# Kernel optimization log

Measured on AMD Instinct MI355X. Metric: run time of the kernel, lower is better.

The kernel has to match this reference:

```python
import jax, jax.numpy as jnp
import numpy as np


def setup_inputs() -> dict:
    key = jax.random.key(0)
    B, T, H, W = 256, 16, 160, 160
    sms = 2
    N = T * (H // sms) * (W // sms)  # 102400 tokens per sample
    k1, _ = jax.random.split(key)
    soft_scores = jax.random.uniform(k1, (B, N), dtype=jnp.float32)
    image_grid_thw = jnp.tile(jnp.array([T, H, W], dtype=jnp.int64), (B, 1))
    return {
        "soft_scores": soft_scores,
        "image_grid_thw": image_grid_thw,
        "spatial_merge_size": sms,
    }


def reference(soft_scores, image_grid_thw, spatial_merge_size,
              lambda_compact=1.0, lambda_tv=1.0, eps=1e-6):
    if soft_scores.ndim == 3:
        soft_scores = soft_scores[..., 0]
    B = soft_scores.shape[0]
    # Uniform grid across the batch (static shapes) -> vectorize over B.
    thw = np.asarray(image_grid_thw)
    t = int(thw[0, 0])
    h = int(thw[0, 1]) // spatial_merge_size
    w = int(thw[0, 2]) // spatial_merge_size
    n = t * h * w

    # s: [B, t, h, w], clamped at 0 like torch clamp_min(0.0)
    s = jnp.maximum(soft_scores[:, :n].astype(jnp.float32).reshape(B, t, h, w), 0.0)
    tot = jnp.maximum(s.sum(axis=(1, 2, 3), keepdims=True), eps)
    p = s / tot  # per-sample normalized distribution

    yy = jnp.linspace(-1.0, 1.0, h, dtype=jnp.float32).reshape(1, 1, h, 1)
    xx = jnp.linspace(-1.0, 1.0, w, dtype=jnp.float32).reshape(1, 1, 1, w)
    mu_x = (p * xx).sum(axis=(1, 2, 3)).reshape(B, 1, 1, 1)
    mu_y = (p * yy).sum(axis=(1, 2, 3)).reshape(B, 1, 1, 1)
    compact = (p * ((xx - mu_x) ** 2 + (yy - mu_y) ** 2)).sum(axis=(1, 2, 3))  # [B]

    tv = jnp.zeros((B,), dtype=jnp.float32)
    if h > 1:
        tv = tv + jnp.abs(s[:, :, 1:, :] - s[:, :, :-1, :]).mean(axis=(1, 2, 3))
    if w > 1:
        tv = tv + jnp.abs(s[:, :, :, 1:] - s[:, :, :, :-1]).mean(axis=(1, 2, 3))
    if t > 1:
        tv = tv + 0.3 * jnp.abs(s[:, 1:, :, :] - s[:, :-1, :, :]).mean(axis=(1, 2, 3))

    return compact.mean() * lambda_compact + tv.mean() * lambda_tv
```

## Files before the change

kernel.cpp:

```cpp
#include <hip/hip_runtime.h>

#define T_DIM 16
#define H2 80
#define W2 80
#define SLICE (H2 * W2)
#define SAMPLE (T_DIM * SLICE)
#define BANDS 5
#define ROWS_PER_BAND (H2 / BANDS)
#define BLOCK (ROWS_PER_BAND * W2 / 4)

__global__ __launch_bounds__(BLOCK) void tsr_phase1(const float* __restrict__ scores,
                                                    float* __restrict__ ws) {
    __shared__ float lds[(ROWS_PER_BAND + 1) * W2];
    __shared__ float red[(BLOCK / 64) * 7];

    const int blk  = blockIdx.x;
    const int b    = blk / BANDS;
    const int band = blk % BANDS;
    const int tid  = threadIdx.x;

    const int y0  = band * ROWS_PER_BAND;
    const int r   = tid / (W2 / 4);
    const int cx  = tid % (W2 / 4);
    const int y   = y0 + r;
    const int xb  = cx * 4;
    const int pos = tid * 4;

    const float step = 2.0f / (float)(H2 - 1);
    const float yy  = -1.0f + (float)y * step;
    const float xx0 = -1.0f + (float)(xb + 0) * step;
    const float xx1 = -1.0f + (float)(xb + 1) * step;
    const float xx2 = -1.0f + (float)(xb + 2) * step;
    const float xx3 = -1.0f + (float)(xb + 3) * step;
    const float yy2 = yy * yy;
    const float cq0 = xx0 * xx0 + yy2;
    const float cq1 = xx1 * xx1 + yy2;
    const float cq2 = xx2 * xx2 + yy2;
    const float cq3 = xx3 * xx3 + yy2;

    const float4* base = (const float4*)(scores + (size_t)b * SAMPLE);
    const int f4idx = band * BLOCK + tid;
    const bool halo = (y0 + ROWS_PER_BAND < H2) && (tid < W2 / 4);
    const int haloIdx = (y0 + ROWS_PER_BAND) * (W2 / 4) + tid;

    const bool wavail = (xb + 4 < W2);
    const bool havail = (y + 1 < H2);

    float s0 = 0.f, sx = 0.f, sy = 0.f, sq = 0.f;
    float tvh = 0.f, tvw = 0.f, tvt = 0.f;
    float4 prev = make_float4(0.f, 0.f, 0.f, 0.f);

    for (int t = 0; t < T_DIM; ++t) {
        const float4* sl = base + (size_t)t * (SLICE / 4);
        float4 v = sl[f4idx];
        v.x = fmaxf(v.x, 0.f); v.y = fmaxf(v.y, 0.f);
        v.z = fmaxf(v.z, 0.f); v.w = fmaxf(v.w, 0.f);
        float4 hv;
        if (halo) {
            hv = sl[haloIdx];
            hv.x = fmaxf(hv.x, 0.f); hv.y = fmaxf(hv.y, 0.f);
            hv.z = fmaxf(hv.z, 0.f); hv.w = fmaxf(hv.w, 0.f);
        }
        __syncthreads();
        *(float4*)&lds[pos] = v;
        if (halo) *(float4*)&lds[ROWS_PER_BAND * W2 + tid * 4] = hv;
        __syncthreads();

        const float rs = v.x + v.y + v.z + v.w;
        s0 += rs;
        sy = fmaf(yy, rs, sy);
        sx = fmaf(xx0, v.x, sx); sx = fmaf(xx1, v.y, sx);
        sx = fmaf(xx2, v.z, sx); sx = fmaf(xx3, v.w, sx);
        sq = fmaf(cq0, v.x, sq); sq = fmaf(cq1, v.y, sq);
        sq = fmaf(cq2, v.z, sq); sq = fmaf(cq3, v.w, sq);

        tvw += fabsf(v.y - v.x) + fabsf(v.z - v.y) + fabsf(v.w - v.z);
        if (wavail) tvw += fabsf(lds[pos + 4] - v.w);

        if (havail) {
            const float4 d = *(const float4*)&lds[pos + W2];
            tvh += fabsf(d.x - v.x) + fabsf(d.y - v.y) +
                   fabsf(d.z - v.z) + fabsf(d.w - v.w);
        }

        if (t > 0) {
            tvt += fabsf(v.x - prev.x) + fabsf(v.y - prev.y) +
                   fabsf(v.z - prev.z) + fabsf(v.w - prev.w);
        }
        prev = v;
    }

    float acc[7] = {s0, sx, sy, sq, tvh, tvw, tvt};
#pragma unroll
    for (int off = 32; off > 0; off >>= 1) {
#pragma unroll
        for (int i = 0; i < 7; ++i) acc[i] += __shfl_down(acc[i], off);
    }
    const int wave = tid >> 6;
    const int lane = tid & 63;
    __syncthreads();
    if (lane == 0) {
#pragma unroll
        for (int i = 0; i < 7; ++i) red[wave * 7 + i] = acc[i];
    }
    __syncthreads();
    if (tid < 7) {
        float v = 0.f;
#pragma unroll
        for (int wv = 0; wv < BLOCK / 64; ++wv) v += red[wv * 7 + tid];
        atomicAdd(&ws[b * 8 + tid], v);
    }
}

__global__ __launch_bounds__(256) void tsr_finalize(const float* __restrict__ ws,
                                                    float* __restrict__ out, int B) {
    __shared__ float red[256];
    const int tid = threadIdx.x;
    float acc = 0.f;
    const float ch = 1.0f / (float)(T_DIM * (H2 - 1) * W2);
    const float cw = 1.0f / (float)(T_DIM * H2 * (W2 - 1));
    const float ct = 0.3f / (float)((T_DIM - 1) * H2 * W2);
    for (int b = tid; b < B; b += 256) {
        const float* w = ws + b * 8;
        const float S0 = w[0], Sx = w[1], Sy = w[2], Sq = w[3];
        const float Th = w[4], Tw = w[5], Tt = w[6];
        const float tot = fmaxf(S0, 1e-6f);
        const float inv = 1.0f / tot;
        const float mux = Sx * inv, muy = Sy * inv;
        const float m2 = mux * mux + muy * muy;
        const float compact = Sq * inv - 2.0f * m2 + m2 * (S0 * inv);
        const float tv = Th * ch + Tw * cw + Tt * ct;
        acc += compact + tv;
    }
    red[tid] = acc;
    __syncthreads();
    for (int s = 128; s > 0; s >>= 1) {
        if (tid < s) red[tid] += red[tid + s];
        __syncthreads();
    }
    if (tid == 0) out[0] = red[0] / (float)B;
}

extern "C" void kernel_launch(void* const* d_in, const int* in_sizes, int n_in,
                              void* d_out, int out_size, void* d_ws, size_t ws_size,
                              hipStream_t stream) {
    const float* scores = (const float*)d_in[0];
    const int B = in_sizes[0] / SAMPLE;
    float* ws = (float*)d_ws;

    hipMemsetAsync(ws, 0, (size_t)B * 8 * sizeof(float), stream);

    tsr_phase1<<<B * BANDS, BLOCK, 0, stream>>>(scores, ws);
    tsr_finalize<<<1, 256, 0, stream>>>(ws, (float*)d_out, B);
}
```

Measured before the change: 161.7 us.

## Prefetch next time slice in registers and replace atomics with per-block partials

The main loop now loads the next time slice's float4 (and its halo row) before processing the current one. This overlaps global-memory latency with the LDS exchange and arithmetic. Per-block partial sums are written to distinct workspace slots instead of being accumulated with atomicAdd, which removes the memset launch. The finalize kernel sums the five band partials per sample. The cost is more live registers and a larger workspace (B*BANDS*8 floats).

```diff
diff --git a/kernel.cpp b/kernel.cpp
--- a/kernel.cpp
+++ b/kernel.cpp
@@ -8,6 +8,12 @@
 #define BANDS 5
 #define ROWS_PER_BAND (H2 / BANDS)
 #define BLOCK (ROWS_PER_BAND * W2 / 4)
+
+__device__ __forceinline__ float4 relu4(float4 v) {
+    v.x = fmaxf(v.x, 0.f); v.y = fmaxf(v.y, 0.f);
+    v.z = fmaxf(v.z, 0.f); v.w = fmaxf(v.w, 0.f);
+    return v;
+}
 
 __global__ __launch_bounds__(BLOCK) void tsr_phase1(const float* __restrict__ scores,
                                                     float* __restrict__ ws) {
@@ -50,17 +56,19 @@
     float tvh = 0.f, tvw = 0.f, tvt = 0.f;
     float4 prev = make_float4(0.f, 0.f, 0.f, 0.f);
 
+    float4 v = relu4(base[f4idx]);
+    float4 hv = make_float4(0.f, 0.f, 0.f, 0.f);
+    if (halo) hv = relu4(base[haloIdx]);
+
     for (int t = 0; t < T_DIM; ++t) {
-        const float4* sl = base + (size_t)t * (SLICE / 4);
-        float4 v = sl[f4idx];
-        v.x = fmaxf(v.x, 0.f); v.y = fmaxf(v.y, 0.f);
-        v.z = fmaxf(v.z, 0.f); v.w = fmaxf(v.w, 0.f);
-        float4 hv;
-        if (halo) {
-            hv = sl[haloIdx];
-            hv.x = fmaxf(hv.x, 0.f); hv.y = fmaxf(hv.y, 0.f);
-            hv.z = fmaxf(hv.z, 0.f); hv.w = fmaxf(hv.w, 0.f);
+        float4 vn = make_float4(0.f, 0.f, 0.f, 0.f);
+        float4 hvn = make_float4(0.f, 0.f, 0.f, 0.f);
+        if (t + 1 < T_DIM) {
+            const float4* sln = base + (size_t)(t + 1) * (SLICE / 4);
+            vn = sln[f4idx];
+            if (halo) hvn = sln[haloIdx];
         }
+
         __syncthreads();
         *(float4*)&lds[pos] = v;
         if (halo) *(float4*)&lds[ROWS_PER_BAND * W2 + tid * 4] = hv;
@@ -88,6 +96,9 @@
                    fabsf(v.z - prev.z) + fabsf(v.w - prev.w);
         }
         prev = v;
+
+        v = relu4(vn);
+        if (halo) hv = relu4(hvn);
     }
 
     float acc[7] = {s0, sx, sy, sq, tvh, tvw, tvt};
@@ -105,10 +116,10 @@
     }
     __syncthreads();
     if (tid < 7) {
-        float v = 0.f;
+        float s = 0.f;
 #pragma unroll
-        for (int wv = 0; wv < BLOCK / 64; ++wv) v += red[wv * 7 + tid];
-        atomicAdd(&ws[b * 8 + tid], v);
+        for (int wv = 0; wv < BLOCK / 64; ++wv) s += red[wv * 7 + tid];
+        ws[blk * 8 + tid] = s;
     }
 }
 
@@ -121,9 +132,14 @@
     const float cw = 1.0f / (float)(T_DIM * H2 * (W2 - 1));
     const float ct = 0.3f / (float)((T_DIM - 1) * H2 * W2);
     for (int b = tid; b < B; b += 256) {
-        const float* w = ws + b * 8;
-        const float S0 = w[0], Sx = w[1], Sy = w[2], Sq = w[3];
-        const float Th = w[4], Tw = w[5], Tt = w[6];
+        float p[7] = {0.f, 0.f, 0.f, 0.f, 0.f, 0.f, 0.f};
+        for (int band = 0; band < BANDS; ++band) {
+            const float* w = ws + (size_t)(b * BANDS + band) * 8;
+#pragma unroll
+            for (int i = 0; i < 7; ++i) p[i] += w[i];
+        }
+        const float S0 = p[0], Sx = p[1], Sy = p[2], Sq = p[3];
+        const float Th = p[4], Tw = p[5], Tt = p[6];
         const float tot = fmaxf(S0, 1e-6f);
         const float inv = 1.0f / tot;
         const float mux = Sx * inv, muy = Sy * inv;
@@ -148,8 +164,6 @@
     const int B = in_sizes[0] / SAMPLE;
     float* ws = (float*)d_ws;
 
-    hipMemsetAsync(ws, 0, (size_t)B * 8 * sizeof(float), stream);
-
     tsr_phase1<<<B * BANDS, BLOCK, 0, stream>>>(scores, ws);
     tsr_finalize<<<1, 256, 0, stream>>>(ws, (float*)d_out, B);
 }
```

Measured after the change: 160.0 us. No clear change (-1.0%).
